# Performance work log

Hardware: AMD Instinct MI355X
Metric: run time of the kernel (lower is better)

## Reference

```python
import jax, jax.numpy as jnp
import numpy as np
from jax import lax

NDIMS = 3
NUM_SCALES = 3
WINDOW_SIZE = 9
POOL_K = 3


def box_filter(x, win):
    """Separable mean (box) filter, kernel=ones/win^3, same padding. x: [N,C,D,H,W]."""
    pad = win // 2
    for ax in range(NDIMS):
        kshape = [1, 1] + [1] * NDIMS
        kshape[2 + ax] = win
        k = jnp.ones(kshape, x.dtype) / win
        padding = [(pad, pad) if i == ax else (0, 0) for i in range(NDIMS)]
        x = lax.conv_general_dilated(x, k, window_strides=(1,) * NDIMS,
                                     padding=padding,
                                     dimension_numbers=('NCDHW', 'OIDHW', 'NCDHW'))
    return x


def avg_pool3d(x, k=POOL_K, stride=2):
    """avg_pool3d with count_include_pad=False."""
    pad = k // 2
    window = (1, 1, k, k, k)
    strides = (1, 1, stride, stride, stride)
    padding = ((0, 0), (0, 0), (pad, pad), (pad, pad), (pad, pad))
    s = lax.reduce_window(x, jnp.array(0, x.dtype), lax.add, window, strides, padding)
    cnt = lax.reduce_window(jnp.ones_like(x), jnp.array(0, x.dtype), lax.add,
                            window, strides, padding)
    return s / cnt


def single_scale_ncc(Ii, Ji, win):
    mu1 = box_filter(Ii, win)
    mu2 = box_filter(Ji, win)
    sigma1_sq = box_filter(Ii * Ii, win) - mu1 * mu1
    sigma2_sq = box_filter(Ji * Ji, win) - mu2 * mu2
    sigma12 = box_filter(Ii * Ji, win) - mu1 * mu2
    eps = jnp.finfo(sigma12.dtype).eps
    cc = sigma12 * sigma12 / jnp.maximum(sigma1_sq * sigma2_sq, eps)
    return -jnp.mean(cc)


def setup_inputs() -> dict:
    key = jax.random.key(0)
    k1, k2 = jax.random.split(key)
    shape = (2, 1, 160, 192, 160)
    I = jax.random.uniform(k1, shape, dtype=jnp.float32)
    J = jax.random.uniform(k2, shape, dtype=jnp.float32)
    return {"I": I, "J": J}


def reference(I, J):
    # Multi-scale NCC: losses at windows 9/7/5 on pyramid built by stride-2 avg pooling.
    total = jnp.zeros((), I.dtype)
    for i in range(NUM_SCALES):
        # SingleScaleNCC(pred=I, target=J): Ii=target, Ji=pred (symmetric metric)
        total = total + single_scale_ncc(J, I, WINDOW_SIZE - 2 * i) / NUM_SCALES
        if i < NUM_SCALES - 1:
            I = avg_pool3d(I)
            J = avg_pool3d(J)
    return total
```

## Files before the change

kernel.cpp:

```cpp
#include <hip/hip_runtime.h>

#define NCC_EPS 1.1920929e-07f

template<int WIN>
__global__ __launch_bounds__(256)
void ncc_strip_kernel(const float* __restrict__ I, const float* __restrict__ J,
                      const float* __restrict__ SLI, const float* __restrict__ SRI,
                      const float* __restrict__ SLJ, const float* __restrict__ SRJ,
                      const float* __restrict__ zerobuf,
                      int D, int H, int W,
                      int tilesH, int tilesW, int chunksD, int chunkLen,
                      double* __restrict__ acc)
{
    constexpr int RAD  = WIN / 2;
    constexpr int TH = 16, TW = 16;
    constexpr int WROWS = TH + 2 * RAD;
    constexpr int PSTR = 68;
    constexpr int QSTR = 24;
    constexpr int OFF  = 4 - RAD;
    constexpr int NWT  = WROWS * 4;
    constexpr float invV = 1.0f / (float)(WIN * WIN * WIN);

    __shared__ __align__(16) float wb0123[2][WROWS * PSTR];
    __shared__ __align__(16) float wb4[2][WROWS * QSTR];
    __shared__ float red[4];

    int bid = blockIdx.x;
    int tw = bid % tilesW; bid /= tilesW;
    int th = bid % tilesH; bid /= tilesH;
    int cd = bid % chunksD; bid /= chunksD;
    int b  = bid;

    const int h0 = th * TH, w0 = tw * TW;
    const int z0 = cd * chunkLen;
    const int z1 = min(z0 + chunkLen, D);

    const size_t plane = (size_t)H * W;

    const int t  = threadIdx.x;
    const int hh = t >> 4, ww = t & 15;
    const bool valid = (w0 + ww) < W;

    const int wr  = t >> 2;
    const int wc4 = t & 3;
    const bool wact = t < NWT;
    const int wbase = w0 + 4 * wc4 - 4;
    const int wghr  = h0 + wr - RAD;

    const float *bI, *bJ;
    long pstr;
    const bool rowOOB = (wghr < 0) || (wghr >= H);
    if (!wact || rowOOB) {
        bI = zerobuf; bJ = zerobuf; pstr = 0;
    } else if (wbase < 0) {
        size_t off = ((size_t)b * D * H + (size_t)wghr) * 16 + (wbase + 4);
        bI = SLI + off; bJ = SLJ + off; pstr = (long)H * 16;
    } else if (wbase + 12 > W) {
        size_t off = ((size_t)b * D * H + (size_t)wghr) * 16 + (wbase - (W - 12));
        bI = SRI + off; bJ = SRJ + off; pstr = (long)H * 16;
    } else {
        size_t off = (size_t)b * D * plane + (size_t)wghr * W + wbase;
        bI = I + off; bJ = J + off; pstr = (long)plane;
    }

    auto load_slice = [&](int z, float (&fi)[12], float (&fj)[12]) {
        if (wact) {
            const bool zok = (z >= 0) && (z < D);
            const float* pI = zok ? (bI + (size_t)((long)z * pstr)) : zerobuf;
            const float* pJ = zok ? (bJ + (size_t)((long)z * pstr)) : zerobuf;
            float4 a0 = *reinterpret_cast<const float4*>(pI);
            float4 a1 = *reinterpret_cast<const float4*>(pI + 4);
            float4 a2 = *reinterpret_cast<const float4*>(pI + 8);
            float4 b0 = *reinterpret_cast<const float4*>(pJ);
            float4 b1 = *reinterpret_cast<const float4*>(pJ + 4);
            float4 b2 = *reinterpret_cast<const float4*>(pJ + 8);
            fi[0]=a0.x; fi[1]=a0.y; fi[2]=a0.z; fi[3]=a0.w;
            fi[4]=a1.x; fi[5]=a1.y; fi[6]=a1.z; fi[7]=a1.w;
            fi[8]=a2.x; fi[9]=a2.y; fi[10]=a2.z; fi[11]=a2.w;
            fj[0]=b0.x; fj[1]=b0.y; fj[2]=b0.z; fj[3]=b0.w;
            fj[4]=b1.x; fj[5]=b1.y; fj[6]=b1.z; fj[7]=b1.w;
            fj[8]=b2.x; fj[9]=b2.y; fj[10]=b2.z; fj[11]=b2.w;
        }
    };

    float ring[WIN][5];
    float rs[5];
    #pragma unroll
    for (int s = 0; s < WIN; ++s)
        #pragma unroll
        for (int c = 0; c < 5; ++c) ring[s][c] = 0.f;
    #pragma unroll
    for (int c = 0; c < 5; ++c) rs[c] = 0.f;

    float ccsum = 0.f;

    float fiC[12], fjC[12], fiN[12], fjN[12];
    const int zend = z1 + RAD;
    load_slice(z0 - RAD, fiC, fjC);

    for (int zb = z0 - RAD; zb < zend; zb += WIN) {
        #pragma unroll
        for (int ph = 0; ph < WIN; ++ph) {
            const int z = zb + ph;
            if (z < zend) {
                load_slice(z + 1, fiN, fjN);

                const int par = (z + 8) & 1;
                float n0, n1, n2, n3, n4;
                if (wact) {
                    float s0 = 0, s1 = 0, s2 = 0, s3 = 0, s4 = 0;
                    #pragma unroll
                    for (int k = 0; k < WIN; ++k) {
                        float a = fiC[OFF + k], bb = fjC[OFF + k];
                        s0 += a; s1 += bb;
                        s2 = fmaf(a, a, s2);
                        s3 = fmaf(bb, bb, s3);
                        s4 = fmaf(a, bb, s4);
                    }
                    float o0[4], o1[4], o2[4], o3[4], o4[4];
                    o0[0]=s0; o1[0]=s1; o2[0]=s2; o3[0]=s3; o4[0]=s4;
                    #pragma unroll
                    for (int m = 1; m < 4; ++m) {
                        float aL = fiC[OFF + m - 1],       bL = fjC[OFF + m - 1];
                        float aR = fiC[OFF + m - 1 + WIN], bR = fjC[OFF + m - 1 + WIN];
                        s0 += aR - aL;
                        s1 += bR - bL;
                        s2 = s2 + aR * aR - aL * aL;
                        s3 = s3 + bR * bR - bL * bL;
                        s4 = s4 + aR * bR - aL * bL;
                        o0[m]=s0; o1[m]=s1; o2[m]=s2; o3[m]=s3; o4[m]=s4;
                    }
                    #pragma unroll
                    for (int m = 0; m < 4; ++m) {
                        *reinterpret_cast<float4*>(&wb0123[par][wr * PSTR + 16 * wc4 + 4 * m]) =
                            make_float4(o0[m], o1[m], o2[m], o3[m]);
                    }
                    *reinterpret_cast<float4*>(&wb4[par][wr * QSTR + 4 * wc4]) =
                        make_float4(o4[0], o4[1], o4[2], o4[3]);
                }
                __builtin_amdgcn_sched_barrier(0);
                asm volatile("s_waitcnt lgkmcnt(0)");
                __builtin_amdgcn_s_barrier();
                __builtin_amdgcn_sched_barrier(0);
                {
                    float4 a4 = make_float4(0.f, 0.f, 0.f, 0.f);
                    float nn4 = 0.f;
                    #pragma unroll
                    for (int dh = 0; dh < WIN; ++dh) {
                        float4 v = *reinterpret_cast<const float4*>(
                            &wb0123[par][(hh + dh) * PSTR + 4 * ww]);
                        a4.x += v.x; a4.y += v.y; a4.z += v.z; a4.w += v.w;
                        nn4 += wb4[par][(hh + dh) * QSTR + ww];
                    }
                    n0 = a4.x; n1 = a4.y; n2 = a4.z; n3 = a4.w; n4 = nn4;
                }
                rs[0] += n0 - ring[ph][0]; ring[ph][0] = n0;
                rs[1] += n1 - ring[ph][1]; ring[ph][1] = n1;
                rs[2] += n2 - ring[ph][2]; ring[ph][2] = n2;
                rs[3] += n3 - ring[ph][3]; ring[ph][3] = n3;
                rs[4] += n4 - ring[ph][4]; ring[ph][4] = n4;

                const int zo = z - RAD;
                if (valid && zo >= z0) {
                    float muI = rs[0] * invV;
                    float muJ = rs[1] * invV;
                    float sII = rs[2] * invV - muI * muI;
                    float sJJ = rs[3] * invV - muJ * muJ;
                    float s12 = rs[4] * invV - muI * muJ;
                    float cc = (s12 * s12) / fmaxf(sII * sJJ, NCC_EPS);
                    ccsum += cc;
                }
                #pragma unroll
                for (int e = 0; e < 12; ++e) { fiC[e] = fiN[e]; fjC[e] = fjN[e]; }
            }
        }
    }

    for (int off = 32; off > 0; off >>= 1)
        ccsum += __shfl_down(ccsum, off);
    const int wid = t >> 6, lane = t & 63;
    if (lane == 0) red[wid] = ccsum;
    __syncthreads();
    if (t == 0) {
        float s = red[0] + red[1] + red[2] + red[3];
        atomicAdd(acc, (double)s);
    }
}

__global__ void strip_fill(const float* __restrict__ I, const float* __restrict__ J,
                           float* __restrict__ SLI, float* __restrict__ SRI,
                           float* __restrict__ SLJ, float* __restrict__ SRJ,
                           int D, int H, int W, int N1)
{
    int idx = blockIdx.x * 256 + threadIdx.x;
    if (idx >= 4 * N1) return;
    int bufid = idx / N1;
    int r = idx - bufid * N1;
    int c4 = r & 3; r >>= 2;
    int h = r % H; int zb = r / H;

    const float* in = (bufid >= 2) ? J : I;
    float* out = (bufid == 0) ? SLI : (bufid == 1) ? SRI : (bufid == 2) ? SLJ : SRJ;
    const bool right = bufid & 1;
    const int c0 = 4 * c4 + (right ? (W - 12) : -4);

    float4 v = make_float4(0.f, 0.f, 0.f, 0.f);
    if (c0 >= 0 && c0 + 4 <= W)
        v = *reinterpret_cast<const float4*>(in + ((size_t)zb * H + h) * W + c0);
    *reinterpret_cast<float4*>(out + ((size_t)zb * H + h) * 16 + 4 * c4) = v;
}

template<int WIN>
__global__ __launch_bounds__(256)
void ncc_pad_kernel(const float* __restrict__ Pi, const float* __restrict__ Pj,
                    int Dp, int Hp, int Wp, int Dreal, int Wreal,
                    int tilesH, int tilesW, int chunksD, int chunkLen,
                    double* __restrict__ acc)
{
    constexpr int RAD  = WIN / 2;
    constexpr int TH = 16, TW = 16;
    constexpr int WROWS = TH + 2 * RAD;
    constexpr int PSTR = 68;
    constexpr int QSTR = 24;
    constexpr int OFF  = 4 - RAD;
    constexpr int NWT  = WROWS * 4;
    constexpr float invV = 1.0f / (float)(WIN * WIN * WIN);

    __shared__ __align__(16) float wb0123[2][WROWS * PSTR];
    __shared__ __align__(16) float wb4[2][WROWS * QSTR];
    __shared__ float red[4];

    int bid = blockIdx.x;
    int tw = bid % tilesW; bid /= tilesW;
    int th = bid % tilesH; bid /= tilesH;
    int cd = bid % chunksD; bid /= chunksD;
    int b  = bid;

    const int h0 = th * TH, w0 = tw * TW;
    const int z0 = cd * chunkLen;
    const int z1 = min(z0 + chunkLen, Dreal);

    const size_t plane = (size_t)Hp * Wp;
    const float* Ib = Pi + (size_t)b * Dp * plane;
    const float* Jb = Pj + (size_t)b * Dp * plane;

    const int t  = threadIdx.x;
    const int hh = t >> 4, ww = t & 15;
    const bool valid = (w0 + ww) < Wreal;

    const int wr  = t >> 2;
    const int wc4 = t & 3;
    const bool wact = t < NWT;
    const size_t rowoff = (size_t)(h0 + wr) * Wp + (w0 + 4 * wc4);

    auto load_slice = [&](int zp, float (&fi)[12], float (&fj)[12]) {
        if (wact) {
            const float* rI = Ib + (size_t)zp * plane + rowoff;
            const float* rJ = Jb + (size_t)zp * plane + rowoff;
            float4 a0 = *reinterpret_cast<const float4*>(rI);
            float4 a1 = *reinterpret_cast<const float4*>(rI + 4);
            float4 a2 = *reinterpret_cast<const float4*>(rI + 8);
            float4 b0 = *reinterpret_cast<const float4*>(rJ);
            float4 b1 = *reinterpret_cast<const float4*>(rJ + 4);
            float4 b2 = *reinterpret_cast<const float4*>(rJ + 8);
            fi[0]=a0.x; fi[1]=a0.y; fi[2]=a0.z; fi[3]=a0.w;
            fi[4]=a1.x; fi[5]=a1.y; fi[6]=a1.z; fi[7]=a1.w;
            fi[8]=a2.x; fi[9]=a2.y; fi[10]=a2.z; fi[11]=a2.w;
            fj[0]=b0.x; fj[1]=b0.y; fj[2]=b0.z; fj[3]=b0.w;
            fj[4]=b1.x; fj[5]=b1.y; fj[6]=b1.z; fj[7]=b1.w;
            fj[8]=b2.x; fj[9]=b2.y; fj[10]=b2.z; fj[11]=b2.w;
        }
    };

    float ring[WIN][5];
    float rs[5];
    #pragma unroll
    for (int s = 0; s < WIN; ++s)
        #pragma unroll
        for (int c = 0; c < 5; ++c) ring[s][c] = 0.f;
    #pragma unroll
    for (int c = 0; c < 5; ++c) rs[c] = 0.f;

    float ccsum = 0.f;

    float fiC[12], fjC[12], fiN[12], fjN[12];
    const int zend = z1 + RAD;
    load_slice(z0 - RAD + 4, fiC, fjC);

    for (int zb = z0 - RAD; zb < zend; zb += WIN) {
        #pragma unroll
        for (int ph = 0; ph < WIN; ++ph) {
            const int z = zb + ph;
            if (z < zend) {
                const int zpn = min(z + 5, Dp - 1);
                load_slice(zpn, fiN, fjN);

                const int par = (z + 4) & 1;
                float n0, n1, n2, n3, n4;
                if (wact) {
                    float s0 = 0, s1 = 0, s2 = 0, s3 = 0, s4 = 0;
                    #pragma unroll
                    for (int k = 0; k < WIN; ++k) {
                        float a = fiC[OFF + k], bb = fjC[OFF + k];
                        s0 += a; s1 += bb;
                        s2 = fmaf(a, a, s2);
                        s3 = fmaf(bb, bb, s3);
                        s4 = fmaf(a, bb, s4);
                    }
                    float o0[4], o1[4], o2[4], o3[4], o4[4];
                    o0[0]=s0; o1[0]=s1; o2[0]=s2; o3[0]=s3; o4[0]=s4;
                    #pragma unroll
                    for (int m = 1; m < 4; ++m) {
                        float aL = fiC[OFF + m - 1],       bL = fjC[OFF + m - 1];
                        float aR = fiC[OFF + m - 1 + WIN], bR = fjC[OFF + m - 1 + WIN];
                        s0 += aR - aL;
                        s1 += bR - bL;
                        s2 = s2 + aR * aR - aL * aL;
                        s3 = s3 + bR * bR - bL * bL;
                        s4 = s4 + aR * bR - aL * bL;
                        o0[m]=s0; o1[m]=s1; o2[m]=s2; o3[m]=s3; o4[m]=s4;
                    }
                    #pragma unroll
                    for (int m = 0; m < 4; ++m) {
                        *reinterpret_cast<float4*>(&wb0123[par][wr * PSTR + 16 * wc4 + 4 * m]) =
                            make_float4(o0[m], o1[m], o2[m], o3[m]);
                    }
                    *reinterpret_cast<float4*>(&wb4[par][wr * QSTR + 4 * wc4]) =
                        make_float4(o4[0], o4[1], o4[2], o4[3]);
                }
                __builtin_amdgcn_sched_barrier(0);
                asm volatile("s_waitcnt lgkmcnt(0)");
                __builtin_amdgcn_s_barrier();
                __builtin_amdgcn_sched_barrier(0);
                {
                    float4 a4 = make_float4(0.f, 0.f, 0.f, 0.f);
                    float nn4 = 0.f;
                    #pragma unroll
                    for (int dh = 0; dh < WIN; ++dh) {
                        float4 v = *reinterpret_cast<const float4*>(
                            &wb0123[par][(hh + dh) * PSTR + 4 * ww]);
                        a4.x += v.x; a4.y += v.y; a4.z += v.z; a4.w += v.w;
                        nn4 += wb4[par][(hh + dh) * QSTR + ww];
                    }
                    n0 = a4.x; n1 = a4.y; n2 = a4.z; n3 = a4.w; n4 = nn4;
                }
                rs[0] += n0 - ring[ph][0]; ring[ph][0] = n0;
                rs[1] += n1 - ring[ph][1]; ring[ph][1] = n1;
                rs[2] += n2 - ring[ph][2]; ring[ph][2] = n2;
                rs[3] += n3 - ring[ph][3]; ring[ph][3] = n3;
                rs[4] += n4 - ring[ph][4]; ring[ph][4] = n4;

                const int zo = z - RAD;
                if (valid && zo >= z0) {
                    float muI = rs[0] * invV;
                    float muJ = rs[1] * invV;
                    float sII = rs[2] * invV - muI * muI;
                    float sJJ = rs[3] * invV - muJ * muJ;
                    float s12 = rs[4] * invV - muI * muJ;
                    float cc = (s12 * s12) / fmaxf(sII * sJJ, NCC_EPS);
                    ccsum += cc;
                }
                #pragma unroll
                for (int e = 0; e < 12; ++e) { fiC[e] = fiN[e]; fjC[e] = fjN[e]; }
            }
        }
    }

    for (int off = 32; off > 0; off >>= 1)
        ccsum += __shfl_down(ccsum, off);
    const int wid = t >> 6, lane = t & 63;
    if (lane == 0) red[wid] = ccsum;
    __syncthreads();
    if (t == 0) {
        float s = red[0] + red[1] + red[2] + red[3];
        atomicAdd(acc, (double)s);
    }
}

__global__ void pool_b2p_kernel(const float* __restrict__ inA, const float* __restrict__ inB,
                                float* __restrict__ outA, float* __restrict__ outB,
                                int D, int H, int W, int oD, int oH, int oW,
                                int oDp, int oHp, int oWp, int total)
{
    int idx0 = blockIdx.x * 256 + threadIdx.x;
    if (idx0 >= 2 * total) return;
    const bool isB = idx0 >= total;
    int idx = isB ? idx0 - total : idx0;
    const float* in = isB ? inB : inA;
    float* out = isB ? outB : outA;

    int ow = idx % oW; int tmp = idx / oW;
    int oh = tmp % oH; tmp /= oH;
    int od = tmp % oD; int b = tmp / oD;

    int dlo = max(2 * od - 1, 0), dhi = min(2 * od + 2, D);
    int hlo = max(2 * oh - 1, 0), hhi = min(2 * oh + 2, H);
    int wlo = max(2 * ow - 1, 0), whi = min(2 * ow + 2, W);

    const float* ib = in + (size_t)b * D * H * W;
    float s = 0.f;
    for (int d = dlo; d < dhi; ++d)
        for (int h = hlo; h < hhi; ++h)
            for (int w = wlo; w < whi; ++w)
                s += ib[((size_t)d * H + h) * W + w];
    int cnt = (dhi - dlo) * (hhi - hlo) * (whi - wlo);
    out[((size_t)(b * oDp + od + 4) * oHp + (oh + 4)) * oWp + (ow + 4)] = s / (float)cnt;
}

__global__ void pool_pad_kernel(const float* __restrict__ inA, const float* __restrict__ inB,
                                float* __restrict__ outA, float* __restrict__ outB,
                                int D, int H, int W, int iDp, int iHp, int iWp,
                                int oD, int oH, int oW, int oDp, int oHp, int oWp,
                                int total)
{
    int idx0 = blockIdx.x * 256 + threadIdx.x;
    if (idx0 >= 2 * total) return;
    const bool isB = idx0 >= total;
    int idx = isB ? idx0 - total : idx0;
    const float* in = isB ? inB : inA;
    float* out = isB ? outB : outA;

    int ow = idx % oW; int tmp = idx / oW;
    int oh = tmp % oH; tmp /= oH;
    int od = tmp % oD; int b = tmp / oD;

    const size_t ip = (size_t)iHp * iWp;
    const float* ib = in + (size_t)b * iDp * ip;
    float s = 0.f;
    #pragma unroll
    for (int dd = 0; dd < 3; ++dd)
        #pragma unroll
        for (int dh = 0; dh < 3; ++dh) {
            const float* r = ib + (size_t)(2 * od + 3 + dd) * ip
                                + (size_t)(2 * oh + 3 + dh) * iWp + (2 * ow + 3);
            s += r[0]; s += r[1]; s += r[2];
        }
    int dlo = max(2 * od - 1, 0), dhi = min(2 * od + 2, D);
    int hlo = max(2 * oh - 1, 0), hhi = min(2 * oh + 2, H);
    int wlo = max(2 * ow - 1, 0), whi = min(2 * ow + 2, W);
    int cnt = (dhi - dlo) * (hhi - hlo) * (whi - wlo);
    out[((size_t)(b * oDp + od + 4) * oHp + (oh + 4)) * oWp + (ow + 4)] = s / (float)cnt;
}

template<int WIN>
__global__ __launch_bounds__(256)
void ncc_scale_kernel(const float* __restrict__ I, const float* __restrict__ J,
                      int D, int H, int W,
                      int tilesH, int tilesW, int chunksD, int chunkLen,
                      double* __restrict__ acc)
{
    constexpr int RAD  = WIN / 2;
    constexpr int TH = 16, TW = 16;
    constexpr int WROWS = TH + 2 * RAD;
    constexpr int PSTR = 68;
    constexpr int QSTR = 24;
    constexpr int OFF  = 4 - RAD;
    constexpr int NWT  = WROWS * 4;
    constexpr float invV = 1.0f / (float)(WIN * WIN * WIN);

    __shared__ __align__(16) float wb0123[2][WROWS * PSTR];
    __shared__ __align__(16) float wb4[2][WROWS * QSTR];
    __shared__ float red[4];

    int bid = blockIdx.x;
    int tw = bid % tilesW; bid /= tilesW;
    int th = bid % tilesH; bid /= tilesH;
    int cd = bid % chunksD; bid /= chunksD;
    int b  = bid;

    const int h0 = th * TH, w0 = tw * TW;
    const int z0 = cd * chunkLen;
    const int z1 = min(z0 + chunkLen, D);

    const size_t plane = (size_t)H * W;
    const float* Ib = I + (size_t)b * D * plane;
    const float* Jb = J + (size_t)b * D * plane;

    const int t  = threadIdx.x;
    const int hh = t >> 4, ww = t & 15;
    const int gh = h0 + hh, gw = w0 + ww;
    const bool valid = (gh < H) && (gw < W);

    const int wr  = t >> 2;
    const int wc4 = t & 3;
    const bool wact = t < NWT;
    const int wbase = w0 + 4 * wc4 - 4;
    const int wghr  = h0 + wr - RAD;

    auto load_slice = [&](int z, float (&fi)[12], float (&fj)[12]) {
        const bool zok = (z >= 0) && (z < D);
        if (zok && wact && wghr >= 0 && wghr < H) {
            const float* rowI = Ib + (size_t)z * plane + (size_t)wghr * W;
            const float* rowJ = Jb + (size_t)z * plane + (size_t)wghr * W;
            if (wbase >= 0 && wbase + 12 <= W) {
                float4 a0 = *reinterpret_cast<const float4*>(rowI + wbase);
                float4 a1 = *reinterpret_cast<const float4*>(rowI + wbase + 4);
                float4 a2 = *reinterpret_cast<const float4*>(rowI + wbase + 8);
                float4 b0 = *reinterpret_cast<const float4*>(rowJ + wbase);
                float4 b1 = *reinterpret_cast<const float4*>(rowJ + wbase + 4);
                float4 b2 = *reinterpret_cast<const float4*>(rowJ + wbase + 8);
                fi[0]=a0.x; fi[1]=a0.y; fi[2]=a0.z; fi[3]=a0.w;
                fi[4]=a1.x; fi[5]=a1.y; fi[6]=a1.z; fi[7]=a1.w;
                fi[8]=a2.x; fi[9]=a2.y; fi[10]=a2.z; fi[11]=a2.w;
                fj[0]=b0.x; fj[1]=b0.y; fj[2]=b0.z; fj[3]=b0.w;
                fj[4]=b1.x; fj[5]=b1.y; fj[6]=b1.z; fj[7]=b1.w;
                fj[8]=b2.x; fj[9]=b2.y; fj[10]=b2.z; fj[11]=b2.w;
            } else {
                #pragma unroll
                for (int e = 0; e < 12; ++e) {
                    int cg = wbase + e;
                    bool ok = (cg >= 0) && (cg < W);
                    fi[e] = ok ? rowI[cg] : 0.f;
                    fj[e] = ok ? rowJ[cg] : 0.f;
                }
// ... 74 lines not shown
                rs[0] += n0 - ring[ph][0]; ring[ph][0] = n0;
                rs[1] += n1 - ring[ph][1]; ring[ph][1] = n1;
                rs[2] += n2 - ring[ph][2]; ring[ph][2] = n2;
                rs[3] += n3 - ring[ph][3]; ring[ph][3] = n3;
                rs[4] += n4 - ring[ph][4]; ring[ph][4] = n4;

                const int zo = z - RAD;
                if (valid && zo >= z0) {
                    float muI = rs[0] * invV;
                    float muJ = rs[1] * invV;
                    float sII = rs[2] * invV - muI * muI;
                    float sJJ = rs[3] * invV - muJ * muJ;
                    float s12 = rs[4] * invV - muI * muJ;
                    float cc = (s12 * s12) / fmaxf(sII * sJJ, NCC_EPS);
                    ccsum += cc;
                }
                #pragma unroll
                for (int e = 0; e < 12; ++e) { fiC[e] = fiN[e]; fjC[e] = fjN[e]; }
            }
        }
    }

    for (int off = 32; off > 0; off >>= 1)
        ccsum += __shfl_down(ccsum, off);
    const int wid = t >> 6, lane = t & 63;
    if (lane == 0) red[wid] = ccsum;
    __syncthreads();
    if (t == 0) {
        float s = red[0] + red[1] + red[2] + red[3];
        atomicAdd(acc, (double)s);
    }
}

__global__ void pool_kernel2(const float* __restrict__ inA, const float* __restrict__ inB,
                             float* __restrict__ outA, float* __restrict__ outB,
                             int D, int H, int W, int oD, int oH, int oW, int total)
{
    int idx0 = blockIdx.x * 256 + threadIdx.x;
    if (idx0 >= 2 * total) return;
    const bool isB = idx0 >= total;
    int idx = isB ? idx0 - total : idx0;
    const float* in = isB ? inB : inA;
    float* out = isB ? outB : outA;

    int ow = idx % oW; int tmp = idx / oW;
    int oh = tmp % oH; tmp /= oH;
    int od = tmp % oD; int b = tmp / oD;

    int dlo = max(2 * od - 1, 0), dhi = min(2 * od + 2, D);
    int hlo = max(2 * oh - 1, 0), hhi = min(2 * oh + 2, H);
    int wlo = max(2 * ow - 1, 0), whi = min(2 * ow + 2, W);

    const float* ib = in + (size_t)b * D * H * W;
    float s = 0.f;
    for (int d = dlo; d < dhi; ++d)
        for (int h = hlo; h < hhi; ++h)
            for (int w = wlo; w < whi; ++w)
                s += ib[((size_t)d * H + h) * W + w];
    int cnt = (dhi - dlo) * (hhi - hlo) * (whi - wlo);
    out[idx] = s / (float)cnt;
}

__global__ void finalize_kernel(const double* __restrict__ acc, float* __restrict__ out)
{
    double m = acc[0] / 9830400.0 + acc[1] / 1228800.0 + acc[2] / 153600.0;
    out[0] = (float)(-m / 3.0);
}

extern "C" void kernel_launch(void* const* d_in, const int* in_sizes, int n_in,
                              void* d_out, int out_size, void* d_ws, size_t ws_size,
                              hipStream_t stream)
{
    const float* I0 = (const float*)d_in[0];
    const float* J0 = (const float*)d_in[1];
    float* out = (float*)d_out;

    char* ws = (char*)d_ws;
    float* zerobuf = (float*)ws;
    double* acc = (double*)(ws + 192);

    const size_t SSZ  = (size_t)2 * 160 * 192 * 16;
    const size_t P1SZ = (size_t)2 * 88 * 104 * 88;
    const size_t P2SZ = (size_t)2 * 48 * 56 * 56;
    const size_t need = 256 + (4 * SSZ + 2 * P1SZ + 2 * P2SZ) * sizeof(float);

    if (ws_size >= need) {
        float* SLI = (float*)(ws + 256);
        float* SRI = SLI + SSZ;
        float* SLJ = SRI + SSZ;
        float* SRJ = SLJ + SSZ;
        float* P1I = SRJ + SSZ;
        float* P1J = P1I + P1SZ;
        float* P2I = P1J + P1SZ;
        float* P2J = P2I + P2SZ;

        hipMemsetAsync(ws, 0, 256, stream);
        hipMemsetAsync(P1I, 0, (2 * P1SZ + 2 * P2SZ) * sizeof(float), stream);

        {
            int N1 = 2 * 160 * 192 * 4;
            int blocks = (4 * N1 + 255) / 256;
            strip_fill<<<blocks, 256, 0, stream>>>(I0, J0, SLI, SRI, SLJ, SRJ,
                                                   160, 192, 160, N1);
        }
        ncc_strip_kernel<9><<<2 * 12 * 10 * 4, 256, 0, stream>>>(
            I0, J0, SLI, SRI, SLJ, SRJ, zerobuf,
            160, 192, 160, 12, 10, 4, 40, acc + 0);
        {
            int total = 2 * 80 * 96 * 80;
            int blocks = (2 * total + 255) / 256;
            pool_b2p_kernel<<<blocks, 256, 0, stream>>>(I0, J0, P1I, P1J,
                                                        160, 192, 160, 80, 96, 80,
                                                        88, 104, 88, total);
        }
        ncc_pad_kernel<7><<<2 * 6 * 5 * 4, 256, 0, stream>>>(
            P1I, P1J, 88, 104, 88, 80, 80, 6, 5, 4, 20, acc + 1);
        {
            int total = 2 * 40 * 48 * 40;
            int blocks = (2 * total + 255) / 256;
            pool_pad_kernel<<<blocks, 256, 0, stream>>>(P1I, P1J, P2I, P2J,
                                                        80, 96, 80, 88, 104, 88,
                                                        40, 48, 40, 48, 56, 56, total);
        }
        ncc_pad_kernel<5><<<2 * 3 * 3 * 5, 256, 0, stream>>>(
            P2I, P2J, 48, 56, 56, 40, 40, 3, 3, 5, 8, acc + 2);
    } else {
        hipMemsetAsync(ws, 0, 256, stream);
        float* I1 = (float*)(ws + 256);
        float* J1 = I1 + (size_t)2 * 80 * 96 * 80;
        float* I2 = J1 + (size_t)2 * 80 * 96 * 80;
        float* J2 = I2 + (size_t)2 * 40 * 48 * 40;

        ncc_scale_kernel<9><<<2 * 12 * 10 * 4, 256, 0, stream>>>(
            I0, J0, 160, 192, 160, 12, 10, 4, 40, acc + 0);
        {
            int total = 2 * 80 * 96 * 80;
            int blocks = (2 * total + 255) / 256;
            pool_kernel2<<<blocks, 256, 0, stream>>>(I0, J0, I1, J1,
                                                     160, 192, 160, 80, 96, 80, total);
        }
        ncc_scale_kernel<7><<<2 * 6 * 5 * 8, 256, 0, stream>>>(
            I1, J1, 80, 96, 80, 6, 5, 8, 10, acc + 1);
        {
            int total = 2 * 40 * 48 * 40;
            int blocks = (2 * total + 255) / 256;
            pool_kernel2<<<blocks, 256, 0, stream>>>(I1, J1, I2, J2,
                                                     80, 96, 80, 40, 48, 40, total);
        }
        ncc_scale_kernel<5><<<2 * 3 * 3 * 14, 256, 0, stream>>>(
            I2, J2, 40, 48, 40, 3, 3, 14, 3, acc + 2);
    }

    finalize_kernel<<<1, 1, 0, stream>>>(acc, out);
}
```

Measured before the change: 201.8 us.

## Split scale-0 NCC into interior and edge kernels, drop strip buffers

Removes the strip_fill pre-pass and its side buffers. Scale 0 is now handled by an interior kernel that reads the raw inputs with no boundary selection, plus an edge-only kernel that runs the bounds-checked path on the outer ring of tiles. Depth chunking is also retuned at every scale to launch more blocks. This is meant to cut an extra kernel launch and its memory traffic, and to take boundary-check overhead out of most tiles, at the cost of two launches for scale 0.

```diff
diff --git a/kernel.cpp b/kernel.cpp
--- a/kernel.cpp
+++ b/kernel.cpp
@@ -4,216 +4,8 @@
 
 template<int WIN>
 __global__ __launch_bounds__(256)
-void ncc_strip_kernel(const float* __restrict__ I, const float* __restrict__ J,
-                      const float* __restrict__ SLI, const float* __restrict__ SRI,
-                      const float* __restrict__ SLJ, const float* __restrict__ SRJ,
-                      const float* __restrict__ zerobuf,
-                      int D, int H, int W,
-                      int tilesH, int tilesW, int chunksD, int chunkLen,
-                      double* __restrict__ acc)
-{
-    constexpr int RAD  = WIN / 2;
-    constexpr int TH = 16, TW = 16;
-    constexpr int WROWS = TH + 2 * RAD;
-    constexpr int PSTR = 68;
-    constexpr int QSTR = 24;
-    constexpr int OFF  = 4 - RAD;
-    constexpr int NWT  = WROWS * 4;
-    constexpr float invV = 1.0f / (float)(WIN * WIN * WIN);
-
-    __shared__ __align__(16) float wb0123[2][WROWS * PSTR];
-    __shared__ __align__(16) float wb4[2][WROWS * QSTR];
-    __shared__ float red[4];
-
-    int bid = blockIdx.x;
-    int tw = bid % tilesW; bid /= tilesW;
-    int th = bid % tilesH; bid /= tilesH;
-    int cd = bid % chunksD; bid /= chunksD;
-    int b  = bid;
-
-    const int h0 = th * TH, w0 = tw * TW;
-    const int z0 = cd * chunkLen;
-    const int z1 = min(z0 + chunkLen, D);
-
-    const size_t plane = (size_t)H * W;
-
-    const int t  = threadIdx.x;
-    const int hh = t >> 4, ww = t & 15;
-    const bool valid = (w0 + ww) < W;
-
-    const int wr  = t >> 2;
-    const int wc4 = t & 3;
-    const bool wact = t < NWT;
-    const int wbase = w0 + 4 * wc4 - 4;
-    const int wghr  = h0 + wr - RAD;
-
-    const float *bI, *bJ;
-    long pstr;
-    const bool rowOOB = (wghr < 0) || (wghr >= H);
-    if (!wact || rowOOB) {
-        bI = zerobuf; bJ = zerobuf; pstr = 0;
-    } else if (wbase < 0) {
-        size_t off = ((size_t)b * D * H + (size_t)wghr) * 16 + (wbase + 4);
-        bI = SLI + off; bJ = SLJ + off; pstr = (long)H * 16;
-    } else if (wbase + 12 > W) {
-        size_t off = ((size_t)b * D * H + (size_t)wghr) * 16 + (wbase - (W - 12));
-        bI = SRI + off; bJ = SRJ + off; pstr = (long)H * 16;
-    } else {
-        size_t off = (size_t)b * D * plane + (size_t)wghr * W + wbase;
-        bI = I + off; bJ = J + off; pstr = (long)plane;
-    }
-
-    auto load_slice = [&](int z, float (&fi)[12], float (&fj)[12]) {
-        if (wact) {
-            const bool zok = (z >= 0) && (z < D);
-            const float* pI = zok ? (bI + (size_t)((long)z * pstr)) : zerobuf;
-            const float* pJ = zok ? (bJ + (size_t)((long)z * pstr)) : zerobuf;
-            float4 a0 = *reinterpret_cast<const float4*>(pI);
-            float4 a1 = *reinterpret_cast<const float4*>(pI + 4);
-            float4 a2 = *reinterpret_cast<const float4*>(pI + 8);
-            float4 b0 = *reinterpret_cast<const float4*>(pJ);
-            float4 b1 = *reinterpret_cast<const float4*>(pJ + 4);
-            float4 b2 = *reinterpret_cast<const float4*>(pJ + 8);
-            fi[0]=a0.x; fi[1]=a0.y; fi[2]=a0.z; fi[3]=a0.w;
-            fi[4]=a1.x; fi[5]=a1.y; fi[6]=a1.z; fi[7]=a1.w;
-            fi[8]=a2.x; fi[9]=a2.y; fi[10]=a2.z; fi[11]=a2.w;
-            fj[0]=b0.x; fj[1]=b0.y; fj[2]=b0.z; fj[3]=b0.w;
-            fj[4]=b1.x; fj[5]=b1.y; fj[6]=b1.z; fj[7]=b1.w;
-            fj[8]=b2.x; fj[9]=b2.y; fj[10]=b2.z; fj[11]=b2.w;
-        }
-    };
-
-    float ring[WIN][5];
-    float rs[5];
-    #pragma unroll
-    for (int s = 0; s < WIN; ++s)
-        #pragma unroll
-        for (int c = 0; c < 5; ++c) ring[s][c] = 0.f;
-    #pragma unroll
-    for (int c = 0; c < 5; ++c) rs[c] = 0.f;
-
-    float ccsum = 0.f;
-
-    float fiC[12], fjC[12], fiN[12], fjN[12];
-    const int zend = z1 + RAD;
-    load_slice(z0 - RAD, fiC, fjC);
-
-    for (int zb = z0 - RAD; zb < zend; zb += WIN) {
-        #pragma unroll
-        for (int ph = 0; ph < WIN; ++ph) {
-            const int z = zb + ph;
-            if (z < zend) {
-                load_slice(z + 1, fiN, fjN);
-
-                const int par = (z + 8) & 1;
-                float n0, n1, n2, n3, n4;
-                if (wact) {
-                    float s0 = 0, s1 = 0, s2 = 0, s3 = 0, s4 = 0;
-                    #pragma unroll
-                    for (int k = 0; k < WIN; ++k) {
-                        float a = fiC[OFF + k], bb = fjC[OFF + k];
-                        s0 += a; s1 += bb;
-                        s2 = fmaf(a, a, s2);
-                        s3 = fmaf(bb, bb, s3);
-                        s4 = fmaf(a, bb, s4);
-                    }
-                    float o0[4], o1[4], o2[4], o3[4], o4[4];
-                    o0[0]=s0; o1[0]=s1; o2[0]=s2; o3[0]=s3; o4[0]=s4;
-                    #pragma unroll
-                    for (int m = 1; m < 4; ++m) {
-                        float aL = fiC[OFF + m - 1],       bL = fjC[OFF + m - 1];
-                        float aR = fiC[OFF + m - 1 + WIN], bR = fjC[OFF + m - 1 + WIN];
-                        s0 += aR - aL;
-                        s1 += bR - bL;
-                        s2 = s2 + aR * aR - aL * aL;
-                        s3 = s3 + bR * bR - bL * bL;
-                        s4 = s4 + aR * bR - aL * bL;
-                        o0[m]=s0; o1[m]=s1; o2[m]=s2; o3[m]=s3; o4[m]=s4;
-                    }
-                    #pragma unroll
-                    for (int m = 0; m < 4; ++m) {
-                        *reinterpret_cast<float4*>(&wb0123[par][wr * PSTR + 16 * wc4 + 4 * m]) =
-                            make_float4(o0[m], o1[m], o2[m], o3[m]);
-                    }
-                    *reinterpret_cast<float4*>(&wb4[par][wr * QSTR + 4 * wc4]) =
-                        make_float4(o4[0], o4[1], o4[2], o4[3]);
-                }
-                __builtin_amdgcn_sched_barrier(0);
-                asm volatile("s_waitcnt lgkmcnt(0)");
-                __builtin_amdgcn_s_barrier();
-                __builtin_amdgcn_sched_barrier(0);
-                {
-                    float4 a4 = make_float4(0.f, 0.f, 0.f, 0.f);
-                    float nn4 = 0.f;
-                    #pragma unroll
-                    for (int dh = 0; dh < WIN; ++dh) {
-                        float4 v = *reinterpret_cast<const float4*>(
-                            &wb0123[par][(hh + dh) * PSTR + 4 * ww]);
-                        a4.x += v.x; a4.y += v.y; a4.z += v.z; a4.w += v.w;
-                        nn4 += wb4[par][(hh + dh) * QSTR + ww];
-                    }
-                    n0 = a4.x; n1 = a4.y; n2 = a4.z; n3 = a4.w; n4 = nn4;
-                }
-                rs[0] += n0 - ring[ph][0]; ring[ph][0] = n0;
-                rs[1] += n1 - ring[ph][1]; ring[ph][1] = n1;
-                rs[2] += n2 - ring[ph][2]; ring[ph][2] = n2;
-                rs[3] += n3 - ring[ph][3]; ring[ph][3] = n3;
-                rs[4] += n4 - ring[ph][4]; ring[ph][4] = n4;
-
-                const int zo = z - RAD;
-                if (valid && zo >= z0) {
-                    float muI = rs[0] * invV;
-                    float muJ = rs[1] * invV;
-                    float sII = rs[2] * invV - muI * muI;
-                    float sJJ = rs[3] * invV - muJ * muJ;
-                    float s12 = rs[4] * invV - muI * muJ;
-                    float cc = (s12 * s12) / fmaxf(sII * sJJ, NCC_EPS);
-                    ccsum += cc;
-                }
-                #pragma unroll
-                for (int e = 0; e < 12; ++e) { fiC[e] = fiN[e]; fjC[e] = fjN[e]; }
-            }
-        }
-    }
-
-    for (int off = 32; off > 0; off >>= 1)
-        ccsum += __shfl_down(ccsum, off);
-    const int wid = t >> 6, lane = t & 63;
-    if (lane == 0) red[wid] = ccsum;
-    __syncthreads();
-    if (t == 0) {
-        float s = red[0] + red[1] + red[2] + red[3];
-        atomicAdd(acc, (double)s);
-    }
-}
-
-__global__ void strip_fill(const float* __restrict__ I, const float* __restrict__ J,
-                           float* __restrict__ SLI, float* __restrict__ SRI,
-                           float* __restrict__ SLJ, float* __restrict__ SRJ,
-                           int D, int H, int W, int N1)
-{
-    int idx = blockIdx.x * 256 + threadIdx.x;
-    if (idx >= 4 * N1) return;
-    int bufid = idx / N1;
-    int r = idx - bufid * N1;
-    int c4 = r & 3; r >>= 2;
-    int h = r % H; int zb = r / H;
-
-    const float* in = (bufid >= 2) ? J : I;
-    float* out = (bufid == 0) ? SLI : (bufid == 1) ? SRI : (bufid == 2) ? SLJ : SRJ;
-    const bool right = bufid & 1;
-    const int c0 = 4 * c4 + (right ? (W - 12) : -4);
-
-    float4 v = make_float4(0.f, 0.f, 0.f, 0.f);
-    if (c0 >= 0 && c0 + 4 <= W)
-        v = *reinterpret_cast<const float4*>(in + ((size_t)zb * H + h) * W + c0);
-    *reinterpret_cast<float4*>(out + ((size_t)zb * H + h) * 16 + 4 * c4) = v;
-}
-
-template<int WIN>
-__global__ __launch_bounds__(256)
-void ncc_pad_kernel(const float* __restrict__ Pi, const float* __restrict__ Pj,
-                    int Dp, int Hp, int Wp, int Dreal, int Wreal,
+void ncc_int_kernel(const float* __restrict__ I, const float* __restrict__ J,
+                    int D, int H, int W,
                     int tilesH, int tilesW, int chunksD, int chunkLen,
                     double* __restrict__ acc)
 {
@@ -236,39 +28,43 @@
     int cd = bid % chunksD; bid /= chunksD;
     int b  = bid;
 
-    const int h0 = th * TH, w0 = tw * TW;
+    const int h0 = (th + 1) * TH, w0 = (tw + 1) * TW;
     const int z0 = cd * chunkLen;
-    const int z1 = min(z0 + chunkLen, Dreal);
-
-    const size_t plane = (size_t)Hp * Wp;
-    const float* Ib = Pi + (size_t)b * Dp * plane;
-    const float* Jb = Pj + (size_t)b * Dp * plane;
+    const int z1 = min(z0 + chunkLen, D);
+
+    const size_t plane = (size_t)H * W;
+    const float* Ib = I + (size_t)b * D * plane;
+    const float* Jb = J + (size_t)b * D * plane;
 
     const int t  = threadIdx.x;
     const int hh = t >> 4, ww = t & 15;
-    const bool valid = (w0 + ww) < Wreal;
 
     const int wr  = t >> 2;
     const int wc4 = t & 3;
     const bool wact = t < NWT;
-    const size_t rowoff = (size_t)(h0 + wr) * Wp + (w0 + 4 * wc4);
-
-    auto load_slice = [&](int zp, float (&fi)[12], float (&fj)[12]) {
+    const size_t rowoff = (size_t)(h0 - 4 + wr) * W + (w0 - 4 + 4 * wc4);
+
+    auto load_slice = [&](int z, float (&fi)[12], float (&fj)[12]) {
         if (wact) {
-            const float* rI = Ib + (size_t)zp * plane + rowoff;
-            const float* rJ = Jb + (size_t)zp * plane + rowoff;
-            float4 a0 = *reinterpret_cast<const float4*>(rI);
-            float4 a1 = *reinterpret_cast<const float4*>(rI + 4);
-            float4 a2 = *reinterpret_cast<const float4*>(rI + 8);
-            float4 b0 = *reinterpret_cast<const float4*>(rJ);
-            float4 b1 = *reinterpret_cast<const float4*>(rJ + 4);
-            float4 b2 = *reinterpret_cast<const float4*>(rJ + 8);
-            fi[0]=a0.x; fi[1]=a0.y; fi[2]=a0.z; fi[3]=a0.w;
-            fi[4]=a1.x; fi[5]=a1.y; fi[6]=a1.z; fi[7]=a1.w;
-            fi[8]=a2.x; fi[9]=a2.y; fi[10]=a2.z; fi[11]=a2.w;
-            fj[0]=b0.x; fj[1]=b0.y; fj[2]=b0.z; fj[3]=b0.w;
-            fj[4]=b1.x; fj[5]=b1.y; fj[6]=b1.z; fj[7]=b1.w;
-            fj[8]=b2.x; fj[9]=b2.y; fj[10]=b2.z; fj[11]=b2.w;
+            if (z >= 0 && z < D) {
+                const float* rI = Ib + (size_t)z * plane + rowoff;
+                const float* rJ = Jb + (size_t)z * plane + rowoff;
+                float4 a0 = *reinterpret_cast<const float4*>(rI);
+                float4 a1 = *reinterpret_cast<const float4*>(rI + 4);
+                float4 a2 = *reinterpret_cast<const float4*>(rI + 8);
+                float4 b0 = *reinterpret_cast<const float4*>(rJ);
+                float4 b1 = *reinterpret_cast<const float4*>(rJ + 4);
+                float4 b2 = *reinterpret_cast<const float4*>(rJ + 8);
+                fi[0]=a0.x; fi[1]=a0.y; fi[2]=a0.z; fi[3]=a0.w;
+                fi[4]=a1.x; fi[5]=a1.y; fi[6]=a1.z; fi[7]=a1.w;
+                fi[8]=a2.x; fi[9]=a2.y; fi[10]=a2.z; fi[11]=a2.w;
+                fj[0]=b0.x; fj[1]=b0.y; fj[2]=b0.z; fj[3]=b0.w;
+                fj[4]=b1.x; fj[5]=b1.y; fj[6]=b1.z; fj[7]=b1.w;
+                fj[8]=b2.x; fj[9]=b2.y; fj[10]=b2.z; fj[11]=b2.w;
+            } else {
+                #pragma unroll
+                for (int e = 0; e < 12; ++e) { fi[e] = 0.f; fj[e] = 0.f; }
+            }
         }
     };
 
@@ -285,17 +81,16 @@
 
     float fiC[12], fjC[12], fiN[12], fjN[12];
     const int zend = z1 + RAD;
-    load_slice(z0 - RAD + 4, fiC, fjC);
+    load_slice(z0 - RAD, fiC, fjC);
 
     for (int zb = z0 - RAD; zb < zend; zb += WIN) {
         #pragma unroll
         for (int ph = 0; ph < WIN; ++ph) {
             const int z = zb + ph;
             if (z < zend) {
-                const int zpn = min(z + 5, Dp - 1);
-                load_slice(zpn, fiN, fjN);
-
-                const int par = (z + 4) & 1;
+                load_slice(z + 1, fiN, fjN);
+
+                const int par = (z + 8) & 1;
                 float n0, n1, n2, n3, n4;
                 if (wact) {
                     float s0 = 0, s1 = 0, s2 = 0, s3 = 0, s4 = 0;
@@ -351,7 +146,7 @@
                 rs[4] += n4 - ring[ph][4]; ring[ph][4] = n4;
 
                 const int zo = z - RAD;
-                if (valid && zo >= z0) {
+                if (zo >= z0) {
                     float muI = rs[0] * invV;
                     float muJ = rs[1] * invV;
                     float sII = rs[2] * invV - muI * muI;
@@ -377,72 +172,7 @@
     }
 }
 
-__global__ void pool_b2p_kernel(const float* __restrict__ inA, const float* __restrict__ inB,
-                                float* __restrict__ outA, float* __restrict__ outB,
-                                int D, int H, int W, int oD, int oH, int oW,
-                                int oDp, int oHp, int oWp, int total)
-{
-    int idx0 = blockIdx.x * 256 + threadIdx.x;
-    if (idx0 >= 2 * total) return;
-    const bool isB = idx0 >= total;
-    int idx = isB ? idx0 - total : idx0;
-    const float* in = isB ? inB : inA;
-    float* out = isB ? outB : outA;
-
-    int ow = idx % oW; int tmp = idx / oW;
-    int oh = tmp % oH; tmp /= oH;
-    int od = tmp % oD; int b = tmp / oD;
-
-    int dlo = max(2 * od - 1, 0), dhi = min(2 * od + 2, D);
-    int hlo = max(2 * oh - 1, 0), hhi = min(2 * oh + 2, H);
-    int wlo = max(2 * ow - 1, 0), whi = min(2 * ow + 2, W);
-
-    const float* ib = in + (size_t)b * D * H * W;
-    float s = 0.f;
-    for (int d = dlo; d < dhi; ++d)
-        for (int h = hlo; h < hhi; ++h)
-            for (int w = wlo; w < whi; ++w)
-                s += ib[((size_t)d * H + h) * W + w];
-    int cnt = (dhi - dlo) * (hhi - hlo) * (whi - wlo);
-    out[((size_t)(b * oDp + od + 4) * oHp + (oh + 4)) * oWp + (ow + 4)] = s / (float)cnt;
-}
-
-__global__ void pool_pad_kernel(const float* __restrict__ inA, const float* __restrict__ inB,
-                                float* __restrict__ outA, float* __restrict__ outB,
-                                int D, int H, int W, int iDp, int iHp, int iWp,
-                                int oD, int oH, int oW, int oDp, int oHp, int oWp,
-                                int total)
-{
-    int idx0 = blockIdx.x * 256 + threadIdx.x;
-    if (idx0 >= 2 * total) return;
-    const bool isB = idx0 >= total;
-    int idx = isB ? idx0 - total : idx0;
-    const float* in = isB ? inB : inA;
-    float* out = isB ? outB : outA;
-
-    int ow = idx % oW; int tmp = idx / oW;
-    int oh = tmp % oH; tmp /= oH;
-    int od = tmp % oD; int b = tmp / oD;
-
-    const size_t ip = (size_t)iHp * iWp;
-    const float* ib = in + (size_t)b * iDp * ip;
-    float s = 0.f;
-    #pragma unroll
-    for (int dd = 0; dd < 3; ++dd)
-        #pragma unroll
-        for (int dh = 0; dh < 3; ++dh) {
-            const float* r = ib + (size_t)(2 * od + 3 + dd) * ip
-                                + (size_t)(2 * oh + 3 + dh) * iWp + (2 * ow + 3);
-            s += r[0]; s += r[1]; s += r[2];
-        }
-    int dlo = max(2 * od - 1, 0), dhi = min(2 * od + 2, D);
-    int hlo = max(2 * oh - 1, 0), hhi = min(2 * oh + 2, H);
-    int wlo = max(2 * ow - 1, 0), whi = min(2 * ow + 2, W);
-    int cnt = (dhi - dlo) * (hhi - hlo) * (whi - wlo);
-    out[((size_t)(b * oDp + od + 4) * oHp + (oh + 4)) * oWp + (ow + 4)] = s / (float)cnt;
-}
-
-template<int WIN>
+template<int WIN, bool EDGE>
 __global__ __launch_bounds__(256)
 void ncc_scale_kernel(const float* __restrict__ I, const float* __restrict__ J,
                       int D, int H, int W,
@@ -463,8 +193,17 @@
     __shared__ float red[4];
 
     int bid = blockIdx.x;
-    int tw = bid % tilesW; bid /= tilesW;
-    int th = bid % tilesH; bid /= tilesH;
+    int th, tw;
+    if (EDGE) {
+        int e = bid % 40; bid /= 40;
+        if (e < 12)      { th = e;      tw = 0; }
+        else if (e < 24) { th = e - 12; tw = 9; }
+        else if (e < 32) { th = 0;      tw = e - 24 + 1; }
+        else             { th = 11;     tw = e - 32 + 1; }
+    } else {
+        tw = bid % tilesW; bid /= tilesW;
+        th = bid % tilesH; bid /= tilesH;
+    }
     int cd = bid % chunksD; bid /= chunksD;
     int b  = bid;
 
@@ -478,8 +217,7 @@
 
     const int t  = threadIdx.x;
     const int hh = t >> 4, ww = t & 15;
-    const int gh = h0 + hh, gw = w0 + ww;
-    const bool valid = (gh < H) && (gw < W);
+    const bool valid = (h0 + hh) < H && (w0 + ww) < W;
 
     const int wr  = t >> 2;
     const int wc4 = t & 3;
@@ -620,6 +358,238 @@
     }
 }
 
+template<int WIN>
+__global__ __launch_bounds__(256)
+void ncc_pad_kernel(const float* __restrict__ Pi, const float* __restrict__ Pj,
+                    int Dp, int Hp, int Wp, int Dreal, int Wreal,
+                    int tilesH, int tilesW, int chunksD, int chunkLen,
+                    double* __restrict__ acc)
+{
+    constexpr int RAD  = WIN / 2;
+    constexpr int TH = 16, TW = 16;
+    constexpr int WROWS = TH + 2 * RAD;
+    constexpr int PSTR = 68;
+    constexpr int QSTR = 24;
+    constexpr int OFF  = 4 - RAD;
+    constexpr int NWT  = WROWS * 4;
+    constexpr float invV = 1.0f / (float)(WIN * WIN * WIN);
+
+    __shared__ __align__(16) float wb0123[2][WROWS * PSTR];
+    __shared__ __align__(16) float wb4[2][WROWS * QSTR];
+    __shared__ float red[4];
+
+    int bid = blockIdx.x;
+    int tw = bid % tilesW; bid /= tilesW;
+    int th = bid % tilesH; bid /= tilesH;
+    int cd = bid % chunksD; bid /= chunksD;
+    int b  = bid;
+
+    const int h0 = th * TH, w0 = tw * TW;
+    const int z0 = cd * chunkLen;
+    const int z1 = min(z0 + chunkLen, Dreal);
+
+    const size_t plane = (size_t)Hp * Wp;
+    const float* Ib = Pi + (size_t)b * Dp * plane;
+    const float* Jb = Pj + (size_t)b * Dp * plane;
+
+    const int t  = threadIdx.x;
+    const int hh = t >> 4, ww = t & 15;
+    const bool valid = (w0 + ww) < Wreal;
+
+    const int wr  = t >> 2;
+    const int wc4 = t & 3;
+    const bool wact = t < NWT;
+    const size_t rowoff = (size_t)(h0 + wr) * Wp + (w0 + 4 * wc4);
+
+    auto load_slice = [&](int zp, float (&fi)[12], float (&fj)[12]) {
+        if (wact) {
+            const float* rI = Ib + (size_t)zp * plane + rowoff;
+            const float* rJ = Jb + (size_t)zp * plane + rowoff;
+            float4 a0 = *reinterpret_cast<const float4*>(rI);
+            float4 a1 = *reinterpret_cast<const float4*>(rI + 4);
+            float4 a2 = *reinterpret_cast<const float4*>(rI + 8);
+            float4 b0 = *reinterpret_cast<const float4*>(rJ);
+            float4 b1 = *reinterpret_cast<const float4*>(rJ + 4);
+            float4 b2 = *reinterpret_cast<const float4*>(rJ + 8);
+            fi[0]=a0.x; fi[1]=a0.y; fi[2]=a0.z; fi[3]=a0.w;
+            fi[4]=a1.x; fi[5]=a1.y; fi[6]=a1.z; fi[7]=a1.w;
+            fi[8]=a2.x; fi[9]=a2.y; fi[10]=a2.z; fi[11]=a2.w;
+            fj[0]=b0.x; fj[1]=b0.y; fj[2]=b0.z; fj[3]=b0.w;
+            fj[4]=b1.x; fj[5]=b1.y; fj[6]=b1.z; fj[7]=b1.w;
+            fj[8]=b2.x; fj[9]=b2.y; fj[10]=b2.z; fj[11]=b2.w;
+        }
+    };
+
+    float ring[WIN][5];
+    float rs[5];
+    #pragma unroll
+    for (int s = 0; s < WIN; ++s)
+        #pragma unroll
+        for (int c = 0; c < 5; ++c) ring[s][c] = 0.f;
+    #pragma unroll
+    for (int c = 0; c < 5; ++c) rs[c] = 0.f;
+
+    float ccsum = 0.f;
+
+    float fiC[12], fjC[12], fiN[12], fjN[12];
+    const int zend = z1 + RAD;
+    load_slice(z0 - RAD + 4, fiC, fjC);
+
+    for (int zb = z0 - RAD; zb < zend; zb += WIN) {
+        #pragma unroll
+        for (int ph = 0; ph < WIN; ++ph) {
+            const int z = zb + ph;
+            if (z < zend) {
+                const int zpn = min(z + 5, Dp - 1);
+                load_slice(zpn, fiN, fjN);
+
+                const int par = (z + 4) & 1;
+                float n0, n1, n2, n3, n4;
+                if (wact) {
+                    float s0 = 0, s1 = 0, s2 = 0, s3 = 0, s4 = 0;
+                    #pragma unroll
+                    for (int k = 0; k < WIN; ++k) {
+                        float a = fiC[OFF + k], bb = fjC[OFF + k];
+                        s0 += a; s1 += bb;
+                        s2 = fmaf(a, a, s2);
+                        s3 = fmaf(bb, bb, s3);
+                        s4 = fmaf(a, bb, s4);
+                    }
+                    float o0[4], o1[4], o2[4], o3[4], o4[4];
+                    o0[0]=s0; o1[0]=s1; o2[0]=s2; o3[0]=s3; o4[0]=s4;
+                    #pragma unroll
+                    for (int m = 1; m < 4; ++m) {
+                        float aL = fiC[OFF + m - 1],       bL = fjC[OFF + m - 1];
+                        float aR = fiC[OFF + m - 1 + WIN], bR = fjC[OFF + m - 1 + WIN];
+                        s0 += aR - aL;
+                        s1 += bR - bL;
+                        s2 = s2 + aR * aR - aL * aL;
+                        s3 = s3 + bR * bR - bL * bL;
+                        s4 = s4 + aR * bR - aL * bL;
+                        o0[m]=s0; o1[m]=s1; o2[m]=s2; o3[m]=s3; o4[m]=s4;
+                    }
+                    #pragma unroll
+                    for (int m = 0; m < 4; ++m) {
+                        *reinterpret_cast<float4*>(&wb0123[par][wr * PSTR + 16 * wc4 + 4 * m]) =
+                            make_float4(o0[m], o1[m], o2[m], o3[m]);
+                    }
+                    *reinterpret_cast<float4*>(&wb4[par][wr * QSTR + 4 * wc4]) =
+                        make_float4(o4[0], o4[1], o4[2], o4[3]);
+                }
+                __builtin_amdgcn_sched_barrier(0);
+                asm volatile("s_waitcnt lgkmcnt(0)");
+                __builtin_amdgcn_s_barrier();
+                __builtin_amdgcn_sched_barrier(0);
+                {
+                    float4 a4 = make_float4(0.f, 0.f, 0.f, 0.f);
+                    float nn4 = 0.f;
+                    #pragma unroll
+                    for (int dh = 0; dh < WIN; ++dh) {
+                        float4 v = *reinterpret_cast<const float4*>(
+                            &wb0123[par][(hh + dh) * PSTR + 4 * ww]);
+                        a4.x += v.x; a4.y += v.y; a4.z += v.z; a4.w += v.w;
+                        nn4 += wb4[par][(hh + dh) * QSTR + ww];
+                    }
+                    n0 = a4.x; n1 = a4.y; n2 = a4.z; n3 = a4.w; n4 = nn4;
+                }
+                rs[0] += n0 - ring[ph][0]; ring[ph][0] = n0;
+                rs[1] += n1 - ring[ph][1]; ring[ph][1] = n1;
+                rs[2] += n2 - ring[ph][2]; ring[ph][2] = n2;
+                rs[3] += n3 - ring[ph][3]; ring[ph][3] = n3;
+                rs[4] += n4 - ring[ph][4]; ring[ph][4] = n4;
+
+                const int zo = z - RAD;
+                if (valid && zo >= z0) {
+                    float muI = rs[0] * invV;
+                    float muJ = rs[1] * invV;
+                    float sII = rs[2] * invV - muI * muI;
+                    float sJJ = rs[3] * invV - muJ * muJ;
+                    float s12 = rs[4] * invV - muI * muJ;
+                    float cc = (s12 * s12) / fmaxf(sII * sJJ, NCC_EPS);
+                    ccsum += cc;
+                }
+                #pragma unroll
+                for (int e = 0; e < 12; ++e) { fiC[e] = fiN[e]; fjC[e] = fjN[e]; }
+            }
+        }
+    }
+
+    for (int off = 32; off > 0; off >>= 1)
+        ccsum += __shfl_down(ccsum, off);
+    const int wid = t >> 6, lane = t & 63;
+    if (lane == 0) red[wid] = ccsum;
+    __syncthreads();
+    if (t == 0) {
+        float s = red[0] + red[1] + red[2] + red[3];
+        atomicAdd(acc, (double)s);
+    }
+}
+
+__global__ void pool_b2p_kernel(const float* __restrict__ inA, const float* __restrict__ inB,
+                                float* __restrict__ outA, float* __restrict__ outB,
+                                int D, int H, int W, int oD, int oH, int oW,
+                                int oDp, int oHp, int oWp, int total)
+{
+    int idx0 = blockIdx.x * 256 + threadIdx.x;
+    if (idx0 >= 2 * total) return;
+    const bool isB = idx0 >= total;
+    int idx = isB ? idx0 - total : idx0;
+    const float* in = isB ? inB : inA;
+    float* out = isB ? outB : outA;
+
+    int ow = idx % oW; int tmp = idx / oW;
+    int oh = tmp % oH; tmp /= oH;
+    int od = tmp % oD; int b = tmp / oD;
+
+    int dlo = max(2 * od - 1, 0), dhi = min(2 * od + 2, D);
+    int hlo = max(2 * oh - 1, 0), hhi = min(2 * oh + 2, H);
+    int wlo = max(2 * ow - 1, 0), whi = min(2 * ow + 2, W);
+
+    const float* ib = in + (size_t)b * D * H * W;
+    float s = 0.f;
+    for (int d = dlo; d < dhi; ++d)
+        for (int h = hlo; h < hhi; ++h)
+            for (int w = wlo; w < whi; ++w)
+                s += ib[((size_t)d * H + h) * W + w];
+    int cnt = (dhi - dlo) * (hhi - hlo) * (whi - wlo);
+    out[((size_t)(b * oDp + od + 4) * oHp + (oh + 4)) * oWp + (ow + 4)] = s / (float)cnt;
+}
+
+__global__ void pool_pad_kernel(const float* __restrict__ inA, const float* __restrict__ inB,
+                                float* __restrict__ outA, float* __restrict__ outB,
+                                int D, int H, int W, int iDp, int iHp, int iWp,
+                                int oD, int oH, int oW, int oDp, int oHp, int oWp,
+                                int total)
+{
+    int idx0 = blockIdx.x * 256 + threadIdx.x;
+    if (idx0 >= 2 * total) return;
+    const bool isB = idx0 >= total;
+    int idx = isB ? idx0 - total : idx0;
+    const float* in = isB ? inB : inA;
+    float* out = isB ? outB : outA;
+
+    int ow = idx % oW; int tmp = idx / oW;
+    int oh = tmp % oH; tmp /= oH;
+    int od = tmp % oD; int b = tmp / oD;
+
+    const size_t ip = (size_t)iHp * iWp;
+    const float* ib = in + (size_t)b * iDp * ip;
+    float s = 0.f;
+    #pragma unroll
+    for (int dd = 0; dd < 3; ++dd)
+        #pragma unroll
+        for (int dh = 0; dh < 3; ++dh) {
+            const float* r = ib + (size_t)(2 * od + 3 + dd) * ip
+                                + (size_t)(2 * oh + 3 + dh) * iWp + (2 * ow + 3);
+            s += r[0] + r[1] + r[2];
+        }
+    int dlo = max(2 * od - 1, 0), dhi = min(2 * od + 2, D);
+    int hlo = max(2 * oh - 1, 0), hhi = min(2 * oh + 2, H);
+    int wlo = max(2 * ow - 1, 0), whi = min(2 * ow + 2, W);
+    int cnt = (dhi - dlo) * (hhi - hlo) * (whi - wlo);
+    out[((size_t)(b * oDp + od + 4) * oHp + (oh + 4)) * oWp + (ow + 4)] = s / (float)cnt;
+}
+
 __global__ void pool_kernel2(const float* __restrict__ inA, const float* __restrict__ inB,
                              float* __restrict__ outA, float* __restrict__ outB,
                              int D, int H, int W, int oD, int oH, int oW, int total)
@@ -664,36 +634,25 @@
     float* out = (float*)d_out;
 
     char* ws = (char*)d_ws;
-    float* zerobuf = (float*)ws;
-    double* acc = (double*)(ws + 192);
-
-    const size_t SSZ  = (size_t)2 * 160 * 192 * 16;
+    double* acc = (double*)ws;
+    hipMemsetAsync(acc, 0, 3 * sizeof(double), stream);
+
     const size_t P1SZ = (size_t)2 * 88 * 104 * 88;
     const size_t P2SZ = (size_t)2 * 48 * 56 * 56;
-    const size_t need = 256 + (4 * SSZ + 2 * P1SZ + 2 * P2SZ) * sizeof(float);
+    const size_t need = 256 + (2 * P1SZ + 2 * P2SZ) * sizeof(float);
 
     if (ws_size >= need) {
-        float* SLI = (float*)(ws + 256);
-        float* SRI = SLI + SSZ;
-        float* SLJ = SRI + SSZ;
-        float* SRJ = SLJ + SSZ;
-        float* P1I = SRJ + SSZ;
+        float* P1I = (float*)(ws + 256);
         float* P1J = P1I + P1SZ;
         float* P2I = P1J + P1SZ;
         float* P2J = P2I + P2SZ;
 
-        hipMemsetAsync(ws, 0, 256, stream);
         hipMemsetAsync(P1I, 0, (2 * P1SZ + 2 * P2SZ) * sizeof(float), stream);
 
-        {
-            int N1 = 2 * 160 * 192 * 4;
-            int blocks = (4 * N1 + 255) / 256;
-            strip_fill<<<blocks, 256, 0, stream>>>(I0, J0, SLI, SRI, SLJ, SRJ,
-                                                   160, 192, 160, N1);
-        }
-        ncc_strip_kernel<9><<<2 * 12 * 10 * 4, 256, 0, stream>>>(
-            I0, J0, SLI, SRI, SLJ, SRJ, zerobuf,
-            160, 192, 160, 12, 10, 4, 40, acc + 0);
+        ncc_int_kernel<9><<<2 * 10 * 8 * 6, 256, 0, stream>>>(
+            I0, J0, 160, 192, 160, 10, 8, 6, 27, acc + 0);
+        ncc_scale_kernel<9, true><<<2 * 40 * 6, 256, 0, stream>>>(
+            I0, J0, 160, 192, 160, 12, 10, 6, 27, acc + 0);
         {
             int total = 2 * 80 * 96 * 80;
             int blocks = (2 * total + 255) / 256;
@@ -701,8 +660,8 @@
                                                         160, 192, 160, 80, 96, 80,
                                                         88, 104, 88, total);
         }
-        ncc_pad_kernel<7><<<2 * 6 * 5 * 4, 256, 0, stream>>>(
-            P1I, P1J, 88, 104, 88, 80, 80, 6, 5, 4, 20, acc + 1);
+        ncc_pad_kernel<7><<<2 * 6 * 5 * 10, 256, 0, stream>>>(
+            P1I, P1J, 88, 104, 88, 80, 80, 6, 5, 10, 8, acc + 1);
         {
             int total = 2 * 40 * 48 * 40;
             int blocks = (2 * total + 255) / 256;
@@ -710,33 +669,32 @@
                                                         80, 96, 80, 88, 104, 88,
                                                         40, 48, 40, 48, 56, 56, total);
         }
-        ncc_pad_kernel<5><<<2 * 3 * 3 * 5, 256, 0, stream>>>(
-            P2I, P2J, 48, 56, 56, 40, 40, 3, 3, 5, 8, acc + 2);
+        ncc_pad_kernel<5><<<2 * 3 * 3 * 10, 256, 0, stream>>>(
+            P2I, P2J, 48, 56, 56, 40, 40, 3, 3, 10, 4, acc + 2);
     } else {
-        hipMemsetAsync(ws, 0, 256, stream);
         float* I1 = (float*)(ws + 256);
         float* J1 = I1 + (size_t)2 * 80 * 96 * 80;
         float* I2 = J1 + (size_t)2 * 80 * 96 * 80;
         float* J2 = I2 + (size_t)2 * 40 * 48 * 40;
 
-        ncc_scale_kernel<9><<<2 * 12 * 10 * 4, 256, 0, stream>>>(
-            I0, J0, 160, 192, 160, 12, 10, 4, 40, acc + 0);
+        ncc_scale_kernel<9, false><<<2 * 12 * 10 * 6, 256, 0, stream>>>(
+            I0, J0, 160, 192, 160, 12, 10, 6, 27, acc + 0);
         {
             int total = 2 * 80 * 96 * 80;
             int blocks = (2 * total + 255) / 256;
             pool_kernel2<<<blocks, 256, 0, stream>>>(I0, J0, I1, J1,
                                                      160, 192, 160, 80, 96, 80, total);
         }
-        ncc_scale_kernel<7><<<2 * 6 * 5 * 8, 256, 0, stream>>>(
-            I1, J1, 80, 96, 80, 6, 5, 8, 10, acc + 1);
+        ncc_scale_kernel<7, false><<<2 * 6 * 5 * 10, 256, 0, stream>>>(
+            I1, J1, 80, 96, 80, 6, 5, 10, 8, acc + 1);
         {
             int total = 2 * 40 * 48 * 40;
             int blocks = (2 * total + 255) / 256;
             pool_kernel2<<<blocks, 256, 0, stream>>>(I1, J1, I2, J2,
                                                      80, 96, 80, 40, 48, 40, total);
         }
-        ncc_scale_kernel<5><<<2 * 3 * 3 * 14, 256, 0, stream>>>(
-            I2, J2, 40, 48, 40, 3, 3, 14, 3, acc + 2);
+        ncc_scale_kernel<5, false><<<2 * 3 * 3 * 10, 256, 0, stream>>>(
+            I2, J2, 40, 48, 40, 3, 3, 10, 4, acc + 2);
     }
 
     finalize_kernel<<<1, 1, 0, stream>>>(acc, out);
```

Result: slower. 229.3 us (+13.6%).
